# Kernel tuning notes

Hardware: AMD Instinct MI355X
Metric: run time of the kernel (lower is better)

The kernel has to match this reference:

```python
import jax, jax.numpy as jnp
import numpy as np

NUM_LAYERS = 2
B, T, D, H = 8, 2048, 512, 512


def setup_inputs() -> dict:
    key = jax.random.key(0)
    ks = jax.random.split(key, 12)
    s_in = 1.0 / np.sqrt(D)
    s_h = 1.0 / np.sqrt(H)
    s_p = 1.0 / np.sqrt(2 * H)
    inputs = jax.random.normal(ks[0], (B, T, D), dtype=jnp.float32)
    seq_lengths = jax.random.randint(ks[1], (B,), 1, T + 1, dtype=jnp.int32)
    # per-layer LSTM params, flax convention: input dense no bias, hidden dense with bias
    Wx_f = jax.random.normal(ks[2], (NUM_LAYERS, D, 4 * H), dtype=jnp.float32) * s_in
    Wh_f = jax.random.normal(ks[3], (NUM_LAYERS, H, 4 * H), dtype=jnp.float32) * s_h
    b_f = jnp.zeros((NUM_LAYERS, 4 * H), dtype=jnp.float32)
    Wx_b = jax.random.normal(ks[4], (NUM_LAYERS, D, 4 * H), dtype=jnp.float32) * s_in
    Wh_b = jax.random.normal(ks[5], (NUM_LAYERS, H, 4 * H), dtype=jnp.float32) * s_h
    b_b = jnp.zeros((NUM_LAYERS, 4 * H), dtype=jnp.float32)
    # bidirectional merge projection: concat(fwd,bwd) [2H] -> D
    Wp = jax.random.normal(ks[6], (NUM_LAYERS, 2 * H, D), dtype=jnp.float32) * s_p
    bp = jnp.zeros((NUM_LAYERS, D), dtype=jnp.float32)
    return {
        "inputs": inputs, "seq_lengths": seq_lengths,
        "Wx_f": Wx_f, "Wh_f": Wh_f, "b_f": b_f,
        "Wx_b": Wx_b, "Wh_b": Wh_b, "b_b": b_b,
        "Wp": Wp, "bp": bp,
    }


def flip_sequences(x, seq_lengths):
    # flip only the valid prefix of each sequence; padding stays at the end
    # (matches flax.linen.recurrent.flip_sequences used by nnx.Bidirectional)
    t = jnp.arange(x.shape[1])[None, :]           # [1, T]
    L = seq_lengths[:, None]                      # [B, 1]
    idx = jnp.where(t < L, L - 1 - t, t)          # [B, T]
    return jnp.take_along_axis(x, idx[:, :, None], axis=1)


def lstm(x, Wx, Wh, b):
    # x: [B, T, Din] -> outputs [B, T, H]; zero initial carry
    Bn = x.shape[0]
    Hn = Wh.shape[0]
    xp = jnp.einsum('btd,dg->btg', x, Wx)         # precompute input projections [B,T,4H]

    def step(carry, xt):
        c, h = carry
        g = xt + h @ Wh + b                       # [B, 4H]
        i, f, gg, o = jnp.split(g, 4, axis=-1)
        c = jax.nn.sigmoid(f) * c + jax.nn.sigmoid(i) * jnp.tanh(gg)
        h = jax.nn.sigmoid(o) * jnp.tanh(c)
        return (c, h), h

    c0 = jnp.zeros((Bn, Hn), x.dtype)
    (_, _), ys = jax.lax.scan(step, (c0, c0), jnp.swapaxes(xp, 0, 1))
    return jnp.swapaxes(ys, 0, 1)                 # [B, T, H]


def reference(inputs, seq_lengths, Wx_f, Wh_f, b_f, Wx_b, Wh_b, b_b, Wp, bp):
    x = inputs
    for l in range(NUM_LAYERS):
        yf = lstm(x, Wx_f[l], Wh_f[l], b_f[l])
        xr = flip_sequences(x, seq_lengths)
        yb = flip_sequences(lstm(xr, Wx_b[l], Wh_b[l], b_b[l]), seq_lengths)
        # bidirectional merge projection back to in_features; dropout=0 -> identity
        x = jnp.concatenate([yf, yb], axis=-1) @ Wp[l] + bp[l]
    return x
```

## Files before the change

### kernel.cpp

```cpp
#include <hip/hip_runtime.h>
#include <hip/hip_fp16.h>
#include <math.h>

#define T_LEN 2048
#define NB 8
#define DD 512
#define HH 512
#define G4 2048
#define CAT2H 1024

typedef _Float16 h2_t __attribute__((ext_vector_type(2)));

__device__ __forceinline__ h2_t f2h2(float x, float y) {
  h2_t r; r[0] = (_Float16)x; r[1] = (_Float16)y; return r;
}

__device__ __forceinline__ float4 ld4(const float* p) { return *(const float4*)p; }
__device__ __forceinline__ float4 ld4(const __half* p) {
  const __half2 a = *(const __half2*)p;
  const __half2 b = *(const __half2*)(p + 2);
  return make_float4(__half2float(a.x), __half2float(a.y),
                     __half2float(b.x), __half2float(b.y));
}
__device__ __forceinline__ void st4(float* p, float4 v) { *(float4*)p = v; }
__device__ __forceinline__ void st4(__half* p, float4 v) {
  *(__half2*)p = __floats2half2_rn(v.x, v.y);
  *(__half2*)(p + 2) = __floats2half2_rn(v.z, v.w);
}

template <typename TA, typename TC>
__global__ __launch_bounds__(256) void gemm_bias(
    const TA* __restrict__ A, const float* __restrict__ B0,
    const float* __restrict__ B1, const float* __restrict__ bias0,
    const float* __restrict__ bias1, TC* __restrict__ C0, TC* __restrict__ C1,
    int M, int N, int K) {
  const float* __restrict__ B = blockIdx.y ? B1 : B0;
  const float* __restrict__ bias = blockIdx.y ? bias1 : bias0;
  TC* __restrict__ C = blockIdx.y ? C1 : C0;
  __shared__ h2_t As2[8][132];
  __shared__ h2_t Bs2[8][132];
  const int nTiles = N >> 7;
  const int bx = blockIdx.x % nTiles;
  const int by = blockIdx.x / nTiles;
  const int tid = threadIdx.x;
  const int tx = tid & 15, ty = tid >> 4;
  const TA* Ab = A + (size_t)by * 128 * K;
  const float* Bb = B + ((size_t)bx << 7);
  float acc[8][8];
#pragma unroll
  for (int i = 0; i < 8; i++)
#pragma unroll
    for (int j = 0; j < 8; j++) acc[i][j] = 0.f;

  for (int k0 = 0; k0 < K; k0 += 16) {
    __syncthreads();
#pragma unroll
    for (int i = 0; i < 2; i++) {
      int idx = i * 256 + tid;
      int m = idx >> 2, kv = idx & 3;
      float4 va = ld4(Ab + (size_t)m * K + k0 + kv * 4);
      As2[kv * 2][m] = f2h2(va.x, va.y);
      As2[kv * 2 + 1][m] = f2h2(va.z, va.w);
    }
#pragma unroll
    for (int i = 0; i < 2; i++) {
      int idx = i * 256 + tid;
      int kp = idx >> 6, n0 = (idx & 63) * 2;
      const float* bp0 = Bb + (size_t)(k0 + 2 * kp) * N + n0;
      float2 r0 = *(const float2*)bp0;
      float2 r1 = *(const float2*)(bp0 + N);
      Bs2[kp][n0] = f2h2(r0.x, r1.x);
      Bs2[kp][n0 + 1] = f2h2(r0.y, r1.y);
    }
    __syncthreads();
#pragma unroll
    for (int kp = 0; kp < 8; kp++) {
      h2_t a2[8], b2[8];
      *(float4*)&a2[0] = *(const float4*)&As2[kp][ty * 8];
      *(float4*)&a2[4] = *(const float4*)&As2[kp][ty * 8 + 4];
      *(float4*)&b2[0] = *(const float4*)&Bs2[kp][tx * 8];
      *(float4*)&b2[4] = *(const float4*)&Bs2[kp][tx * 8 + 4];
#pragma unroll
      for (int i = 0; i < 8; i++)
#pragma unroll
        for (int j = 0; j < 8; j++)
          acc[i][j] = __builtin_amdgcn_fdot2(a2[i], b2[j], acc[i][j], false);
    }
  }
  const int row0 = by * 128 + ty * 8;
  const int col0 = bx * 128 + tx * 8;
  float bv[8];
  *(float4*)&bv[0] = *(const float4*)&bias[col0];
  *(float4*)&bv[4] = *(const float4*)&bias[col0 + 4];
#pragma unroll
  for (int i = 0; i < 8; i++) {
    float4 o0 = make_float4(acc[i][0] + bv[0], acc[i][1] + bv[1],
                            acc[i][2] + bv[2], acc[i][3] + bv[3]);
    float4 o1 = make_float4(acc[i][4] + bv[4], acc[i][5] + bv[5],
                            acc[i][6] + bv[6], acc[i][7] + bv[7]);
    st4(&C[(size_t)(row0 + i) * N + col0], o0);
    st4(&C[(size_t)(row0 + i) * N + col0 + 4], o1);
  }
}

__device__ __forceinline__ float sigmf_(float x) {
  return 1.f / (1.f + __expf(-x));
}
__device__ __forceinline__ float tanhf_(float x) {
  return 1.f - 2.f / (1.f + __expf(2.f * x));
}

__global__ __launch_bounds__(512, 2) void lstm_scan(
    const __half* __restrict__ Pf, const __half* __restrict__ Pb,
    const float* __restrict__ Whf, const float* __restrict__ Whb,
    const int* __restrict__ seqlen, __half* __restrict__ cat,
    unsigned long long* hbuf, float* diag, int tagbase) {
  const int w = blockIdx.x;
  const int chain = w & 15;
  const int us = w >> 4;
  const int dir = chain & 1;
  const int b = chain >> 1;
  const int t = threadIdx.x;
  const int col = t & 127;
  const int kc = t >> 7;
  const int C = (col >> 5) * HH + us * 32 + (col & 31);

  const float* __restrict__ Wh = dir ? Whb : Whf;
  const __half* __restrict__ P = dir ? Pb : Pf;
  const int L = seqlen[b];

  __shared__ __half h16[HH];
  __shared__ float partial[4][128];

  h2_t wr2[64];
  {
    const float* wp = Wh + (size_t)(kc * 128) * G4 + C;
#pragma unroll
    for (int j = 0; j < 64; j++)
      wr2[j] = f2h2(wp[(size_t)(2 * j) * G4], wp[(size_t)(2 * j + 1) * G4]);
  }
  float c_state = 0.f;

  unsigned long long* hb_base = hbuf + ((size_t)dir * NB + b) * HH;
  const size_t slotStride = (size_t)2 * NB * HH;
  const unsigned tb = (unsigned)tagbase;

  if (t < 32) {
    __hip_atomic_store(hb_base + us * 32 + t, ((unsigned long long)tb << 32),
                       __ATOMIC_RELAXED, __HIP_MEMORY_SCOPE_AGENT);
  }

  for (int s = 0; s < T_LEN; s++) {
    const int tin = dir ? ((s < L) ? (L - 1 - s) : s) : s;
    float p0 = 0.f, p1 = 0.f, p2 = 0.f, p3 = 0.f;
    if (t < 32) {
      const __half* pr = P + ((size_t)b * T_LEN + tin) * G4 + us * 32 + t;
      p0 = __half2float(pr[0]);
      p1 = __half2float(pr[HH]);
      p2 = __half2float(pr[2 * HH]);
      p3 = __half2float(pr[3 * HH]);
    }

    int dead = 0;
    {
      const unsigned want = tb + (unsigned)s;
      unsigned long long* hp = hb_base + (size_t)(s & 1) * slotStride + t;
      unsigned long long v;
      int tries = 0;
      for (;;) {
        v = __hip_atomic_load(hp, __ATOMIC_RELAXED, __HIP_MEMORY_SCOPE_AGENT);
        if ((unsigned)(v >> 32) == want) break;
        if (++tries > (1 << 20)) { dead = 1; break; }
      }
      h16[t] = __float2half(__uint_as_float((unsigned)v));
    }
    if (__syncthreads_or(dead)) {
      if (t == 0) { atomicAdd(diag + 1, 1.0f); diag[2] = (float)s; }
      break;
    }

    float a0 = 0.f, a1 = 0.f, a2 = 0.f, a3 = 0.f;
    const __half* hk = &h16[kc * 128];
#pragma unroll
    for (int jj = 0; jj < 16; jj++) {
      float4 hv4 = *(const float4*)&hk[jj * 8];
      const h2_t* hp2 = (const h2_t*)&hv4;
      a0 = __builtin_amdgcn_fdot2(hp2[0], wr2[jj * 4 + 0], a0, false);
      a1 = __builtin_amdgcn_fdot2(hp2[1], wr2[jj * 4 + 1], a1, false);
      a2 = __builtin_amdgcn_fdot2(hp2[2], wr2[jj * 4 + 2], a2, false);
      a3 = __builtin_amdgcn_fdot2(hp2[3], wr2[jj * 4 + 3], a3, false);
    }
    partial[kc][col] = (a0 + a1) + (a2 + a3);
    __syncthreads();

    if (t < 32) {
      float g0 = p0, g1 = p1, g2 = p2, g3 = p3;
#pragma unroll
      for (int k2 = 0; k2 < 4; k2++) {
        g0 += partial[k2][t];
        g1 += partial[k2][32 + t];
        g2 += partial[k2][64 + t];
        g3 += partial[k2][96 + t];
      }
      c_state = sigmf_(g1) * c_state + sigmf_(g0) * tanhf_(g2);
      float hn = sigmf_(g3) * tanhf_(c_state);
      unsigned long long pv =
          ((unsigned long long)(tb + (unsigned)s + 1u) << 32) |
          (unsigned long long)__float_as_uint(hn);
      __hip_atomic_store(hb_base + (size_t)((s + 1) & 1) * slotStride + us * 32 + t,
                         pv, __ATOMIC_RELAXED, __HIP_MEMORY_SCOPE_AGENT);
      cat[((size_t)b * T_LEN + tin) * CAT2H + dir * HH + us * 32 + t] =
          __float2half(hn);
    }
  }
}

__global__ void diag_mark(const float* diag, float* out, float code_ws, int wsfail) {
  if (wsfail) { out[0] = code_ws; return; }
  float nd = diag[1];
  if (nd > 0.f) out[0] = 1.0e7f + nd * 1.0e4f + diag[2];
}

extern "C" void kernel_launch(void* const* d_in, const int* in_sizes, int n_in,
                              void* d_out, int out_size, void* d_ws, size_t ws_size,
                              hipStream_t stream) {
  const float* inputs = (const float*)d_in[0];
  const int* seqlen = (const int*)d_in[1];
  const float* Wx_f = (const float*)d_in[2];
  const float* Wh_f = (const float*)d_in[3];
  const float* b_f  = (const float*)d_in[4];
  const float* Wx_b = (const float*)d_in[5];
  const float* Wh_b = (const float*)d_in[6];
  const float* b_b  = (const float*)d_in[7];
  const float* Wp   = (const float*)d_in[8];
  const float* bp   = (const float*)d_in[9];
  float* out = (float*)d_out;

  const size_t oHB = 256;
  const size_t szHB = (size_t)2 * 16 * HH * sizeof(unsigned long long);
  const size_t oPf = oHB + szHB;
  const size_t oPb = oPf + 67108864ull;
  const size_t oCat = oPb + 67108864ull;
  const size_t oX1 = oCat + 33554432ull;
  const size_t need = oX1 + 16777216ull;

  if (ws_size < need) {
    hipMemsetAsync(d_out, 0, (size_t)out_size * sizeof(float), stream);
    float code = 1.0e8f + (float)(ws_size / (1024.0 * 1024.0)) * 10.0f;
    diag_mark<<<1, 1, 0, stream>>>(nullptr, out, code, 1);
    return;
  }
  char* ws = (char*)d_ws;
  float* diag = (float*)ws;
  unsigned long long* hbuf = (unsigned long long*)(ws + oHB);
  __half* Pf = (__half*)(ws + oPf);
  __half* Pb = (__half*)(ws + oPb);
  __half* cat = (__half*)(ws + oCat);
  __half* x1 = (__half*)(ws + oX1);

  hipMemsetAsync(diag, 0, 256, stream);

  const int MM = NB * T_LEN;

  gemm_bias<float, __half>
      <<<dim3((MM / 128) * (G4 / 128), 2), dim3(256), 0, stream>>>(
          inputs, Wx_f, Wx_b, b_f, b_b, Pf, Pb, MM, G4, DD);
  lstm_scan<<<dim3(256), dim3(512), 0, stream>>>(Pf, Pb, Wh_f, Wh_b, seqlen, cat,
                                                 hbuf, diag, 1);
  gemm_bias<__half, __half>
      <<<dim3((MM / 128) * (DD / 128), 1), dim3(256), 0, stream>>>(
          cat, Wp, Wp, bp, bp, x1, x1, MM, DD, CAT2H);

  gemm_bias<__half, __half>
      <<<dim3((MM / 128) * (G4 / 128), 2), dim3(256), 0, stream>>>(
          x1, Wx_f + (size_t)DD * G4, Wx_b + (size_t)DD * G4, b_f + G4, b_b + G4,
          Pf, Pb, MM, G4, DD);
  lstm_scan<<<dim3(256), dim3(512), 0, stream>>>(
      Pf, Pb, Wh_f + (size_t)HH * G4, Wh_b + (size_t)HH * G4, seqlen, cat, hbuf,
      diag, 3000);
  gemm_bias<__half, float>
      <<<dim3((MM / 128) * (DD / 128), 1), dim3(256), 0, stream>>>(
          cat, Wp + (size_t)CAT2H * DD, Wp + (size_t)CAT2H * DD, bp + DD,
          bp + DD, out, out, MM, DD, CAT2H);

  diag_mark<<<1, 1, 0, stream>>>(diag, out, 0.f, 0);
}
```

Baseline: 8.273 ms.

## Reduce LSTM gate partials with wave shuffles instead of shared memory barrier

```diff
diff --git a/kernel.cpp b/kernel.cpp
--- a/kernel.cpp
+++ b/kernel.cpp
@@ -121,23 +121,25 @@
   const int dir = chain & 1;
   const int b = chain >> 1;
   const int t = threadIdx.x;
-  const int col = t & 127;
-  const int kc = t >> 7;
-  const int C = (col >> 5) * HH + us * 32 + (col & 31);
+  const int lane = t & 63;
+  const int u = t >> 4;
+  const int g = (t >> 2) & 3;
+  const int j = t & 3;
+  const int C = g * HH + us * 32 + u;
+  const int isPub = (t & 15) == 0;
 
   const float* __restrict__ Wh = dir ? Whb : Whf;
   const __half* __restrict__ P = dir ? Pb : Pf;
   const int L = seqlen[b];
 
-  __shared__ __half h16[HH];
-  __shared__ float partial[4][128];
+  __shared__ __half h16[2][HH];
 
   h2_t wr2[64];
   {
-    const float* wp = Wh + (size_t)(kc * 128) * G4 + C;
-#pragma unroll
-    for (int j = 0; j < 64; j++)
-      wr2[j] = f2h2(wp[(size_t)(2 * j) * G4], wp[(size_t)(2 * j + 1) * G4]);
+    const float* wp = Wh + (size_t)(j * 128) * G4 + C;
+#pragma unroll
+    for (int m = 0; m < 64; m++)
+      wr2[m] = f2h2(wp[(size_t)(2 * m) * G4], wp[(size_t)(2 * m + 1) * G4]);
   }
   float c_state = 0.f;
 
@@ -145,16 +147,16 @@
   const size_t slotStride = (size_t)2 * NB * HH;
   const unsigned tb = (unsigned)tagbase;
 
-  if (t < 32) {
-    __hip_atomic_store(hb_base + us * 32 + t, ((unsigned long long)tb << 32),
+  if (isPub) {
+    __hip_atomic_store(hb_base + us * 32 + u, ((unsigned long long)tb << 32),
                        __ATOMIC_RELAXED, __HIP_MEMORY_SCOPE_AGENT);
   }
 
   for (int s = 0; s < T_LEN; s++) {
     const int tin = dir ? ((s < L) ? (L - 1 - s) : s) : s;
     float p0 = 0.f, p1 = 0.f, p2 = 0.f, p3 = 0.f;
-    if (t < 32) {
-      const __half* pr = P + ((size_t)b * T_LEN + tin) * G4 + us * 32 + t;
+    if (isPub) {
+      const __half* pr = P + ((size_t)b * T_LEN + tin) * G4 + us * 32 + u;
       p0 = __half2float(pr[0]);
       p1 = __half2float(pr[HH]);
       p2 = __half2float(pr[2 * HH]);
@@ -172,44 +174,45 @@
         if ((unsigned)(v >> 32) == want) break;
         if (++tries > (1 << 20)) { dead = 1; break; }
       }
-      h16[t] = __float2half(__uint_as_float((unsigned)v));
+      h16[s & 1][t] = __float2half(__uint_as_float((unsigned)v));
     }
     if (__syncthreads_or(dead)) {
       if (t == 0) { atomicAdd(diag + 1, 1.0f); diag[2] = (float)s; }
       break;
     }
 
-    float a0 = 0.f, a1 = 0.f, a2 = 0.f, a3 = 0.f;
-    const __half* hk = &h16[kc * 128];
-#pragma unroll
-    for (int jj = 0; jj < 16; jj++) {
-      float4 hv4 = *(const float4*)&hk[jj * 8];
-      const h2_t* hp2 = (const h2_t*)&hv4;
-      a0 = __builtin_amdgcn_fdot2(hp2[0], wr2[jj * 4 + 0], a0, false);
-      a1 = __builtin_amdgcn_fdot2(hp2[1], wr2[jj * 4 + 1], a1, false);
-      a2 = __builtin_amdgcn_fdot2(hp2[2], wr2[jj * 4 + 2], a2, false);
-      a3 = __builtin_amdgcn_fdot2(hp2[3], wr2[jj * 4 + 3], a3, false);
-    }
-    partial[kc][col] = (a0 + a1) + (a2 + a3);
-    __syncthreads();
-
-    if (t < 32) {
-      float g0 = p0, g1 = p1, g2 = p2, g3 = p3;
-#pragma unroll
-      for (int k2 = 0; k2 < 4; k2++) {
-        g0 += partial[k2][t];
-        g1 += partial[k2][32 + t];
-        g2 += partial[k2][64 + t];
-        g3 += partial[k2][96 + t];
+    float a = 0.f;
+    {
+      const __half* hk = &h16[s & 1][j * 128];
+#pragma unroll
+      for (int i = 0; i < 16; i++) {
+        float4 hv4 = *(const float4*)&hk[i * 8];
+        const h2_t* hp2 = (const h2_t*)&hv4;
+        a = __builtin_amdgcn_fdot2(hp2[0], wr2[i * 4 + 0], a, false);
+        a = __builtin_amdgcn_fdot2(hp2[1], wr2[i * 4 + 1], a, false);
+        a = __builtin_amdgcn_fdot2(hp2[2], wr2[i * 4 + 2], a, false);
+        a = __builtin_amdgcn_fdot2(hp2[3], wr2[i * 4 + 3], a, false);
       }
+    }
+    a += __shfl_xor(a, 1, 64);
+    a += __shfl_xor(a, 2, 64);
+    const int base = lane & ~15;
+    float d0 = __shfl(a, base + 0, 64);
+    float d1 = __shfl(a, base + 4, 64);
+    float d2 = __shfl(a, base + 8, 64);
+    float d3 = __shfl(a, base + 12, 64);
+
+    if (isPub) {
+      float g0 = p0 + d0, g1 = p1 + d1, g2 = p2 + d2, g3 = p3 + d3;
       c_state = sigmf_(g1) * c_state + sigmf_(g0) * tanhf_(g2);
       float hn = sigmf_(g3) * tanhf_(c_state);
       unsigned long long pv =
           ((unsigned long long)(tb + (unsigned)s + 1u) << 32) |
           (unsigned long long)__float_as_uint(hn);
-      __hip_atomic_store(hb_base + (size_t)((s + 1) & 1) * slotStride + us * 32 + t,
-                         pv, __ATOMIC_RELAXED, __HIP_MEMORY_SCOPE_AGENT);
-      cat[((size_t)b * T_LEN + tin) * CAT2H + dir * HH + us * 32 + t] =
+      __hip_atomic_store(
+          hb_base + (size_t)((s + 1) & 1) * slotStride + us * 32 + u, pv,
+          __ATOMIC_RELAXED, __HIP_MEMORY_SCOPE_AGENT);
+      cat[((size_t)b * T_LEN + tin) * CAT2H + dir * HH + us * 32 + u] =
           __float2half(hn);
     }
   }
```

Measured after the change: 10.30 ms. 1.24x slower.

## Map LSTM chains onto single XCDs and poll hidden state via L2-local loads

Applied to the files above, without the earlier changes.

```diff
diff --git a/kernel.cpp b/kernel.cpp
--- a/kernel.cpp
+++ b/kernel.cpp
@@ -114,17 +114,51 @@
     const __half* __restrict__ Pf, const __half* __restrict__ Pb,
     const float* __restrict__ Whf, const float* __restrict__ Whb,
     const int* __restrict__ seqlen, __half* __restrict__ cat,
-    unsigned long long* hbuf, float* diag, int tagbase) {
-  const int w = blockIdx.x;
-  const int chain = w & 15;
-  const int us = w >> 4;
-  const int dir = chain & 1;
-  const int b = chain >> 1;
+    unsigned long long* hbuf, unsigned* ctrl, float* diag, int tagbase) {
   const int t = threadIdx.x;
+  __shared__ int s_ci, s_us, s_fast, s_slow, s_abort;
+
+  if (t == 0) {
+    s_slow = 0; s_abort = 0;
+    int xcd = 0;
+    asm volatile("s_getreg_b32 %0, hwreg(HW_REG_XCC_ID)" : "=s"(xcd));
+    xcd &= 7;
+    unsigned ticket = __hip_atomic_fetch_add(&ctrl[xcd], 1u, __ATOMIC_RELAXED,
+                                             __HIP_MEMORY_SCOPE_AGENT);
+    __hip_atomic_fetch_add(&ctrl[8], 1u, __ATOMIC_RELEASE,
+                           __HIP_MEMORY_SCOPE_AGENT);
+    int ok = 1, tr = 0;
+    while (__hip_atomic_load(&ctrl[8], __ATOMIC_ACQUIRE,
+                             __HIP_MEMORY_SCOPE_AGENT) < 256u) {
+      if (++tr > (1 << 22)) { ok = 0; break; }
+    }
+    if (!ok) {
+      s_abort = 1; s_fast = 0; s_ci = blockIdx.x & 15; s_us = blockIdx.x >> 4;
+    } else {
+      int bal = 1;
+      for (int x = 0; x < 8; x++)
+        bal &= (__hip_atomic_load(&ctrl[x], __ATOMIC_RELAXED,
+                                  __HIP_MEMORY_SCOPE_AGENT) == 32u);
+      if (bal && ticket < 32u) {
+        s_ci = xcd * 2 + (int)(ticket >> 4);
+        s_us = (int)(ticket & 15u);
+        s_fast = 1;
+      } else {
+        s_ci = blockIdx.x & 15; s_us = blockIdx.x >> 4; s_fast = 0;
+      }
+    }
+  }
+  __syncthreads();
+  if (s_abort) {
+    if (t == 0) { atomicAdd(diag + 1, 1.0f); diag[2] = 9999.f; }
+    return;
+  }
+  const int ci = s_ci, us = s_us, fastWG = s_fast;
+  const int dir = ci & 1, b = ci >> 1;
+
   const int col = t & 127;
   const int kc = t >> 7;
   const int C = (col >> 5) * HH + us * 32 + (col & 31);
-
   const float* __restrict__ Wh = dir ? Whb : Whf;
   const __half* __restrict__ P = dir ? Pb : Pf;
   const int L = seqlen[b];
@@ -141,13 +175,19 @@
   }
   float c_state = 0.f;
 
-  unsigned long long* hb_base = hbuf + ((size_t)dir * NB + b) * HH;
+  unsigned long long* hb_base = hbuf + (size_t)ci * HH;
   const size_t slotStride = (size_t)2 * NB * HH;
   const unsigned tb = (unsigned)tagbase;
 
   if (t < 32) {
-    __hip_atomic_store(hb_base + us * 32 + t, ((unsigned long long)tb << 32),
-                       __ATOMIC_RELAXED, __HIP_MEMORY_SCOPE_AGENT);
+    unsigned long long pv = ((unsigned long long)tb << 32);
+    unsigned long long* hdst = hb_base + us * 32 + t;
+    if (fastWG)
+      asm volatile("global_store_dwordx2 %0, %1, off sc0" ::"v"(
+                       (unsigned long long)hdst),
+                   "v"(pv)
+                   : "memory");
+    __hip_atomic_store(hdst, pv, __ATOMIC_RELAXED, __HIP_MEMORY_SCOPE_AGENT);
   }
 
   for (int s = 0; s < T_LEN; s++) {
@@ -161,19 +201,31 @@
       p3 = __half2float(pr[3 * HH]);
     }
 
-    int dead = 0;
+    int dead = 0, slowMark = 0;
     {
       const unsigned want = tb + (unsigned)s;
       unsigned long long* hp = hb_base + (size_t)(s & 1) * slotStride + t;
       unsigned long long v;
+      int fastNow = fastWG && !s_slow;
       int tries = 0;
       for (;;) {
-        v = __hip_atomic_load(hp, __ATOMIC_RELAXED, __HIP_MEMORY_SCOPE_AGENT);
+        if (fastNow) {
+          asm volatile(
+              "global_load_dwordx2 %0, %1, off sc0\n\ts_waitcnt vmcnt(0)"
+              : "=v"(v)
+              : "v"((unsigned long long)hp)
+              : "memory");
+        } else {
+          v = __hip_atomic_load(hp, __ATOMIC_RELAXED, __HIP_MEMORY_SCOPE_AGENT);
+        }
         if ((unsigned)(v >> 32) == want) break;
-        if (++tries > (1 << 20)) { dead = 1; break; }
+        ++tries;
+        if (fastNow && tries >= 1024) { fastNow = 0; slowMark = 1; }
+        if (tries > (1 << 20)) { dead = 1; break; }
       }
       h16[t] = __float2half(__uint_as_float((unsigned)v));
     }
+    if (slowMark) s_slow = 1;
     if (__syncthreads_or(dead)) {
       if (t == 0) { atomicAdd(diag + 1, 1.0f); diag[2] = (float)s; }
       break;
@@ -207,8 +259,14 @@
       unsigned long long pv =
           ((unsigned long long)(tb + (unsigned)s + 1u) << 32) |
           (unsigned long long)__float_as_uint(hn);
-      __hip_atomic_store(hb_base + (size_t)((s + 1) & 1) * slotStride + us * 32 + t,
-                         pv, __ATOMIC_RELAXED, __HIP_MEMORY_SCOPE_AGENT);
+      unsigned long long* hdst =
+          hb_base + (size_t)((s + 1) & 1) * slotStride + us * 32 + t;
+      if (fastWG)
+        asm volatile("global_store_dwordx2 %0, %1, off sc0" ::"v"(
+                         (unsigned long long)hdst),
+                     "v"(pv)
+                     : "memory");
+      __hip_atomic_store(hdst, pv, __ATOMIC_RELAXED, __HIP_MEMORY_SCOPE_AGENT);
       cat[((size_t)b * T_LEN + tin) * CAT2H + dir * HH + us * 32 + t] =
           __float2half(hn);
     }
@@ -252,13 +310,15 @@
   }
   char* ws = (char*)d_ws;
   float* diag = (float*)ws;
+  unsigned* ctrl0 = (unsigned*)(ws + 128);
+  unsigned* ctrl1 = (unsigned*)(ws + 192);
   unsigned long long* hbuf = (unsigned long long*)(ws + oHB);
   __half* Pf = (__half*)(ws + oPf);
   __half* Pb = (__half*)(ws + oPb);
   __half* cat = (__half*)(ws + oCat);
   __half* x1 = (__half*)(ws + oX1);
 
-  hipMemsetAsync(diag, 0, 256, stream);
+  hipMemsetAsync(ws, 0, 256, stream);
 
   const int MM = NB * T_LEN;
 
@@ -266,7 +326,7 @@
       <<<dim3((MM / 128) * (G4 / 128), 2), dim3(256), 0, stream>>>(
           inputs, Wx_f, Wx_b, b_f, b_b, Pf, Pb, MM, G4, DD);
   lstm_scan<<<dim3(256), dim3(512), 0, stream>>>(Pf, Pb, Wh_f, Wh_b, seqlen, cat,
-                                                 hbuf, diag, 1);
+                                                 hbuf, ctrl0, diag, 1);
   gemm_bias<__half, __half>
       <<<dim3((MM / 128) * (DD / 128), 1), dim3(256), 0, stream>>>(
           cat, Wp, Wp, bp, bp, x1, x1, MM, DD, CAT2H);
@@ -277,7 +337,7 @@
           Pf, Pb, MM, G4, DD);
   lstm_scan<<<dim3(256), dim3(512), 0, stream>>>(
       Pf, Pb, Wh_f + (size_t)HH * G4, Wh_b + (size_t)HH * G4, seqlen, cat, hbuf,
-      diag, 3000);
+      ctrl1, diag, 3000);
   gemm_bias<__half, float>
       <<<dim3((MM / 128) * (DD / 128), 1), dim3(256), 0, stream>>>(
           cat, Wp + (size_t)CAT2H * DD, Wp + (size_t)CAT2H * DD, bp + DD,
```

After: 9.660 ms. +16.8%, slower.
